# Kernel optimization log

Hardware: AMD Instinct MI355X
Metric: run time of the kernel (lower is better)

Reference implementation:

```python
import jax, jax.numpy as jnp
import numpy as np


def setup_inputs() -> dict:
    key = jax.random.key(0)
    k1, k2, k3, k4, k5 = jax.random.split(key, 5)
    dim, hidden = 64, 128
    x = jax.random.normal(k1, (32, 128, 128, dim), dtype=jnp.float32)
    # torch Linear stores (out,in); we store transposed so y = x @ W + b
    W_expand = jax.random.normal(k2, (dim, hidden), dtype=jnp.float32) * (1.0 / np.sqrt(dim))
    b_expand = jax.random.normal(k3, (hidden,), dtype=jnp.float32) * 0.01
    W_restore = jax.random.normal(k4, (hidden, 1), dtype=jnp.float32) * (1.0 / np.sqrt(hidden))
    b_restore = jax.random.normal(k5, (1,), dtype=jnp.float32) * 0.01
    return {
        "x": x,
        "W_expand": W_expand,
        "b_expand": b_expand,
        "W_restore": W_restore,
        "b_restore": b_restore,
        "kernel_size": 2,
        "stride": 2,
    }


def reference(x, W_expand, b_expand, W_restore, b_restore, kernel_size, stride):
    b, r, c, d = x.shape
    sr = (r - kernel_size) // stride + 1
    sc = (c - kernel_size) // stride + 1
    s = stride  # original code slices stride x stride windows
    # gather all windows at once: (b, sr, s, sc, s, d)
    ri = (jnp.arange(sr) * stride)[:, None] + jnp.arange(s)[None, :]
    ci = (jnp.arange(sc) * stride)[:, None] + jnp.arange(s)[None, :]
    win = x[:, ri[:, :, None, None], ci[None, None, :, :], :]
    # -> (b, sr, sc, s*s, d)
    win = win.transpose(0, 1, 3, 2, 4, 5).reshape(b, sr, sc, s * s, d)
    # tiny MLP attention weights per window element
    h = jnp.tanh(jnp.einsum('bqpwd,dh->bqpwh', win, W_expand) + b_expand)
    logit = jax.nn.sigmoid(jnp.einsum('bqpwh,ho->bqpwo', h, W_restore)[..., 0] + b_restore[0])
    w = jax.nn.softmax(logit, axis=-1)  # over window elements
    out = jnp.sum(win * w[..., None], axis=3)  # (b, sr, sc, d)
    return out
```

## Files before the change

### kernel.cpp

```cpp
#include <hip/hip_runtime.h>


typedef __attribute__((ext_vector_type(8))) short short8;
typedef __attribute__((ext_vector_type(4))) float floatx4;

#define B_   32
#define R_   128
#define C_   128
#define D_   64
#define H_   128
#define SR_  64
#define SC_  64
#define NW_  (B_ * SR_ * SC_)
#define NGRP_ (NW_ / 4)
#define NBLK_ 2048
#define NWAVE_ (NBLK_ * 4)
#define L_   (NGRP_ / NWAVE_)
#define WTS_ 72

__device__ __forceinline__ unsigned short f2bf(float f) {
  union { float f; unsigned int u; } v; v.f = f;
  unsigned int u = v.u;
  u += 0x7fffu + ((u >> 16) & 1u);
  return (unsigned short)(u >> 16);
}

__device__ __forceinline__ float fast_tanh(float x) {
  float e = __expf(2.0f * x);
  return 1.0f - 2.0f / (e + 1.0f);
}

__global__ __launch_bounds__(256, 2) void softpool_kernel(
    const float* __restrict__ x, const float* __restrict__ We,
    const float* __restrict__ be, const float* __restrict__ Wr,
    const float* __restrict__ br, float* __restrict__ out)
{
  __shared__ __attribute__((aligned(16))) unsigned short WeT[H_ * WTS_];

  const int tid = threadIdx.x;
  for (int idx = tid; idx < D_ * H_; idx += 256) {
    int d = idx >> 7;
    int h = idx & 127;
    WeT[h * WTS_ + d] = f2bf(We[idx]);
  }
  __syncthreads();

  const int lane = tid & 63;
  const int wv   = tid >> 6;
  const int c    = lane & 15;
  const int quad = lane >> 4;

  short8 Bf[8][2];
#pragma unroll
  for (int n = 0; n < 8; ++n)
#pragma unroll
    for (int ks = 0; ks < 2; ++ks)
      Bf[n][ks] = *(const short8*)&WeT[(n * 16 + c) * WTS_ + ks * 32 + quad * 8];

  float beL[8], wrL[8];
#pragma unroll
  for (int n = 0; n < 8; ++n) { beL[n] = be[n * 16 + c]; wrL[n] = Wr[n * 16 + c]; }
  const float brS = br[0];

  const int gw = blockIdx.x * 4 + wv;

  for (int it = 0; it < L_; ++it) {
    const int g = gw + it * NWAVE_;

    const int w0   = g * 4 + (c >> 2);
    const int elem = c & 3;
    const int bb = w0 >> 12;
    const int qq = (w0 >> 6) & 63;
    const int pp = w0 & 63;
    const int row = qq * 2 + (elem >> 1);
    const int col = pp * 2 + (elem & 1);
    const float* xp = x + (((bb * R_ + row) * C_ + col) * D_) + quad * 8;
    floatx4 a0 = *(const floatx4*)(xp);
    floatx4 a1 = *(const floatx4*)(xp + 4);
    floatx4 a2 = *(const floatx4*)(xp + 32);
    floatx4 a3 = *(const floatx4*)(xp + 36);

    short8 A0, A1;
    A0[0] = (short)f2bf(a0[0]); A0[1] = (short)f2bf(a0[1]);
    A0[2] = (short)f2bf(a0[2]); A0[3] = (short)f2bf(a0[3]);
    A0[4] = (short)f2bf(a1[0]); A0[5] = (short)f2bf(a1[1]);
    A0[6] = (short)f2bf(a1[2]); A0[7] = (short)f2bf(a1[3]);
    A1[0] = (short)f2bf(a2[0]); A1[1] = (short)f2bf(a2[1]);
    A1[2] = (short)f2bf(a2[2]); A1[3] = (short)f2bf(a2[3]);
    A1[4] = (short)f2bf(a3[0]); A1[5] = (short)f2bf(a3[1]);
    A1[6] = (short)f2bf(a3[2]); A1[7] = (short)f2bf(a3[3]);

    floatx4 acc[8];
#pragma unroll
    for (int n = 0; n < 8; ++n) {
      floatx4 z = {0.f, 0.f, 0.f, 0.f};
      z = __builtin_amdgcn_mfma_f32_16x16x32_bf16(A0, Bf[n][0], z, 0, 0, 0);
      acc[n] = __builtin_amdgcn_mfma_f32_16x16x32_bf16(A1, Bf[n][1], z, 0, 0, 0);
    }

    float p0 = 0.f, p1 = 0.f, p2 = 0.f, p3 = 0.f;
#pragma unroll
    for (int n = 0; n < 8; ++n) {
      p0 += fast_tanh(acc[n][0] + beL[n]) * wrL[n];
      p1 += fast_tanh(acc[n][1] + beL[n]) * wrL[n];
      p2 += fast_tanh(acc[n][2] + beL[n]) * wrL[n];
      p3 += fast_tanh(acc[n][3] + beL[n]) * wrL[n];
    }
#pragma unroll
    for (int m = 1; m < 16; m <<= 1) {
      p0 += __shfl_xor(p0, m, 64);
      p1 += __shfl_xor(p1, m, 64);
      p2 += __shfl_xor(p2, m, 64);
      p3 += __shfl_xor(p3, m, 64);
    }
    float l0 = 1.0f / (1.0f + __expf(-(p0 + brS)));
    float l1 = 1.0f / (1.0f + __expf(-(p1 + brS)));
    float l2 = 1.0f / (1.0f + __expf(-(p2 + brS)));
    float l3 = 1.0f / (1.0f + __expf(-(p3 + brS)));
    float mx = fmaxf(fmaxf(l0, l1), fmaxf(l2, l3));
    float e0 = __expf(l0 - mx), e1 = __expf(l1 - mx);
    float e2 = __expf(l2 - mx), e3 = __expf(l3 - mx);
    float inv = 1.0f / (e0 + e1 + e2 + e3);
    float w0f = e0 * inv, w1f = e1 * inv, w2f = e2 * inv, w3f = e3 * inv;

    const int wq = g * 4 + quad;
    const int b2 = wq >> 12;
    const int q2 = (wq >> 6) & 63;
    const int p2i = wq & 63;
    const float* xw = x + (((b2 * R_ + q2 * 2) * C_ + p2i * 2) * D_) + c * 4;
    floatx4 x0 = *(const floatx4*)(xw);
    floatx4 x1 = *(const floatx4*)(xw + D_);
    floatx4 x2 = *(const floatx4*)(xw + C_ * D_);
    floatx4 x3 = *(const floatx4*)(xw + C_ * D_ + D_);
    floatx4 o = x0 * w0f + x1 * w1f + x2 * w2f + x3 * w3f;
    *(floatx4*)(out + wq * 64 + c * 4) = o;
  }
}

extern "C" void kernel_launch(void* const* d_in, const int* in_sizes, int n_in,
                              void* d_out, int out_size, void* d_ws, size_t ws_size,
                              hipStream_t stream) {
  const float* x  = (const float*)d_in[0];
  const float* We = (const float*)d_in[1];
  const float* be = (const float*)d_in[2];
  const float* Wr = (const float*)d_in[3];
  const float* br = (const float*)d_in[4];
  float* out = (float*)d_out;
  softpool_kernel<<<NBLK_, 256, 0, stream>>>(x, We, be, Wr, br, out);
}
```

Measured before the change: 237.4 us.

## Simplify tanh/sigmoid/softmax math, hoist pooling loads, raise occupancy

Rewrites tanh as 1-2/(exp2+1), folding constants into the bias and weights and using native exp2 and rcp intrinsics. Drops the softmax max-subtraction, which is safe because sigmoid outputs are bounded. Replaces round-to-nearest-even bf16 conversion with cheaper packed round-half-up. Moves the pooling reloads of x before the MFMA so their latency overlaps with compute, and raises launch bounds to 4 blocks per CU. The extra live registers from the early loads could conflict with the higher occupancy target and cause spills.

```diff
diff --git a/kernel.cpp b/kernel.cpp
--- a/kernel.cpp
+++ b/kernel.cpp
@@ -18,19 +18,22 @@
 #define L_   (NGRP_ / NWAVE_)
 #define WTS_ 72
 
-__device__ __forceinline__ unsigned short f2bf(float f) {
+#define L2E_  1.4426950408889634f
+#define T2L_  2.8853900817779268f
+
+__device__ __forceinline__ unsigned short f2bf_rne(float f) {
   union { float f; unsigned int u; } v; v.f = f;
   unsigned int u = v.u;
   u += 0x7fffu + ((u >> 16) & 1u);
   return (unsigned short)(u >> 16);
 }
 
-__device__ __forceinline__ float fast_tanh(float x) {
-  float e = __expf(2.0f * x);
-  return 1.0f - 2.0f / (e + 1.0f);
+__device__ __forceinline__ unsigned int pk_bf16(float lo, float hi) {
+  union { float f; unsigned int u; } a, b; a.f = lo; b.f = hi;
+  return ((a.u + 0x8000u) >> 16) | ((b.u + 0x8000u) & 0xFFFF0000u);
 }
 
-__global__ __launch_bounds__(256, 2) void softpool_kernel(
+__global__ __launch_bounds__(256, 4) void softpool_kernel(
     const float* __restrict__ x, const float* __restrict__ We,
     const float* __restrict__ be, const float* __restrict__ Wr,
     const float* __restrict__ br, float* __restrict__ out)
@@ -41,7 +44,7 @@
   for (int idx = tid; idx < D_ * H_; idx += 256) {
     int d = idx >> 7;
     int h = idx & 127;
-    WeT[h * WTS_ + d] = f2bf(We[idx]);
+    WeT[h * WTS_ + d] = f2bf_rne(We[idx]);
   }
   __syncthreads();
 
@@ -57,10 +60,15 @@
     for (int ks = 0; ks < 2; ++ks)
       Bf[n][ks] = *(const short8*)&WeT[(n * 16 + c) * WTS_ + ks * 32 + quad * 8];
 
-  float beL[8], wrL[8];
+  float beK[8], wr2[8], swr = 0.f;
 #pragma unroll
-  for (int n = 0; n < 8; ++n) { beL[n] = be[n * 16 + c]; wrL[n] = Wr[n * 16 + c]; }
-  const float brS = br[0];
+  for (int n = 0; n < 8; ++n) {
+    float w = Wr[n * 16 + c];
+    beK[n] = be[n * 16 + c] * T2L_;
+    wr2[n] = -2.0f * w;
+    swr += w;
+  }
+  const float brN = -L2E_ * br[0];
 
   const int gw = blockIdx.x * 4 + wv;
 
@@ -75,36 +83,47 @@
     const int row = qq * 2 + (elem >> 1);
     const int col = pp * 2 + (elem & 1);
     const float* xp = x + (((bb * R_ + row) * C_ + col) * D_) + quad * 8;
+
+    const int wq = g * 4 + quad;
+    const int b2 = wq >> 12;
+    const int q2 = (wq >> 6) & 63;
+    const int p2i = wq & 63;
+    const float* xw = x + (((b2 * R_ + q2 * 2) * C_ + p2i * 2) * D_) + c * 4;
+
     floatx4 a0 = *(const floatx4*)(xp);
     floatx4 a1 = *(const floatx4*)(xp + 4);
     floatx4 a2 = *(const floatx4*)(xp + 32);
     floatx4 a3 = *(const floatx4*)(xp + 36);
+    floatx4 x0 = *(const floatx4*)(xw);
+    floatx4 x1 = *(const floatx4*)(xw + D_);
+    floatx4 x2 = *(const floatx4*)(xw + C_ * D_);
+    floatx4 x3 = *(const floatx4*)(xw + C_ * D_ + D_);
 
-    short8 A0, A1;
-    A0[0] = (short)f2bf(a0[0]); A0[1] = (short)f2bf(a0[1]);
-    A0[2] = (short)f2bf(a0[2]); A0[3] = (short)f2bf(a0[3]);
-    A0[4] = (short)f2bf(a1[0]); A0[5] = (short)f2bf(a1[1]);
-    A0[6] = (short)f2bf(a1[2]); A0[7] = (short)f2bf(a1[3]);
-    A1[0] = (short)f2bf(a2[0]); A1[1] = (short)f2bf(a2[1]);
-    A1[2] = (short)f2bf(a2[2]); A1[3] = (short)f2bf(a2[3]);
-    A1[4] = (short)f2bf(a3[0]); A1[5] = (short)f2bf(a3[1]);
-    A1[6] = (short)f2bf(a3[2]); A1[7] = (short)f2bf(a3[3]);
+    union { unsigned int u[4]; short8 v; } A0u, A1u;
+    A0u.u[0] = pk_bf16(a0[0], a0[1]); A0u.u[1] = pk_bf16(a0[2], a0[3]);
+    A0u.u[2] = pk_bf16(a1[0], a1[1]); A0u.u[3] = pk_bf16(a1[2], a1[3]);
+    A1u.u[0] = pk_bf16(a2[0], a2[1]); A1u.u[1] = pk_bf16(a2[2], a2[3]);
+    A1u.u[2] = pk_bf16(a3[0], a3[1]); A1u.u[3] = pk_bf16(a3[2], a3[3]);
 
     floatx4 acc[8];
 #pragma unroll
     for (int n = 0; n < 8; ++n) {
       floatx4 z = {0.f, 0.f, 0.f, 0.f};
-      z = __builtin_amdgcn_mfma_f32_16x16x32_bf16(A0, Bf[n][0], z, 0, 0, 0);
-      acc[n] = __builtin_amdgcn_mfma_f32_16x16x32_bf16(A1, Bf[n][1], z, 0, 0, 0);
+      z = __builtin_amdgcn_mfma_f32_16x16x32_bf16(A0u.v, Bf[n][0], z, 0, 0, 0);
+      acc[n] = __builtin_amdgcn_mfma_f32_16x16x32_bf16(A1u.v, Bf[n][1], z, 0, 0, 0);
     }
 
-    float p0 = 0.f, p1 = 0.f, p2 = 0.f, p3 = 0.f;
+    float p0 = swr, p1 = swr, p2 = swr, p3 = swr;
 #pragma unroll
     for (int n = 0; n < 8; ++n) {
-      p0 += fast_tanh(acc[n][0] + beL[n]) * wrL[n];
-      p1 += fast_tanh(acc[n][1] + beL[n]) * wrL[n];
-      p2 += fast_tanh(acc[n][2] + beL[n]) * wrL[n];
-      p3 += fast_tanh(acc[n][3] + beL[n]) * wrL[n];
+      float e0 = __builtin_amdgcn_exp2f(fmaf(acc[n][0], T2L_, beK[n]));
+      float e1 = __builtin_amdgcn_exp2f(fmaf(acc[n][1], T2L_, beK[n]));
+      float e2 = __builtin_amdgcn_exp2f(fmaf(acc[n][2], T2L_, beK[n]));
+      float e3 = __builtin_amdgcn_exp2f(fmaf(acc[n][3], T2L_, beK[n]));
+      p0 = fmaf(wr2[n], __builtin_amdgcn_rcpf(e0 + 1.0f), p0);
+      p1 = fmaf(wr2[n], __builtin_amdgcn_rcpf(e1 + 1.0f), p1);
+      p2 = fmaf(wr2[n], __builtin_amdgcn_rcpf(e2 + 1.0f), p2);
+      p3 = fmaf(wr2[n], __builtin_amdgcn_rcpf(e3 + 1.0f), p3);
     }
 #pragma unroll
     for (int m = 1; m < 16; m <<= 1) {
@@ -113,25 +132,17 @@
       p2 += __shfl_xor(p2, m, 64);
       p3 += __shfl_xor(p3, m, 64);
     }
-    float l0 = 1.0f / (1.0f + __expf(-(p0 + brS)));
-    float l1 = 1.0f / (1.0f + __expf(-(p1 + brS)));
-    float l2 = 1.0f / (1.0f + __expf(-(p2 + brS)));
-    float l3 = 1.0f / (1.0f + __expf(-(p3 + brS)));
-    float mx = fmaxf(fmaxf(l0, l1), fmaxf(l2, l3));
-    float e0 = __expf(l0 - mx), e1 = __expf(l1 - mx);
-    float e2 = __expf(l2 - mx), e3 = __expf(l3 - mx);
-    float inv = 1.0f / (e0 + e1 + e2 + e3);
-    float w0f = e0 * inv, w1f = e1 * inv, w2f = e2 * inv, w3f = e3 * inv;
+    float l0 = __builtin_amdgcn_rcpf(1.0f + __builtin_amdgcn_exp2f(fmaf(p0, -L2E_, brN)));
+    float l1 = __builtin_amdgcn_rcpf(1.0f + __builtin_amdgcn_exp2f(fmaf(p1, -L2E_, brN)));
+    float l2 = __builtin_amdgcn_rcpf(1.0f + __builtin_amdgcn_exp2f(fmaf(p2, -L2E_, brN)));
+    float l3 = __builtin_amdgcn_rcpf(1.0f + __builtin_amdgcn_exp2f(fmaf(p3, -L2E_, brN)));
+    float s0 = __builtin_amdgcn_exp2f(l0 * L2E_);
+    float s1 = __builtin_amdgcn_exp2f(l1 * L2E_);
+    float s2 = __builtin_amdgcn_exp2f(l2 * L2E_);
+    float s3 = __builtin_amdgcn_exp2f(l3 * L2E_);
+    float inv = __builtin_amdgcn_rcpf(s0 + s1 + s2 + s3);
+    float w0f = s0 * inv, w1f = s1 * inv, w2f = s2 * inv, w3f = s3 * inv;
 
-    const int wq = g * 4 + quad;
-    const int b2 = wq >> 12;
-    const int q2 = (wq >> 6) & 63;
-    const int p2i = wq & 63;
-    const float* xw = x + (((b2 * R_ + q2 * 2) * C_ + p2i * 2) * D_) + c * 4;
-    floatx4 x0 = *(const floatx4*)(xw);
-    floatx4 x1 = *(const floatx4*)(xw + D_);
-    floatx4 x2 = *(const floatx4*)(xw + C_ * D_);
-    floatx4 x3 = *(const floatx4*)(xw + C_ * D_ + D_);
     floatx4 o = x0 * w0f + x1 * w1f + x2 * w2f + x3 * w3f;
     *(floatx4*)(out + wq * 64 + c * 4) = o;
   }
```

Result: slower. 259.7 us (+9.4%).
